# Kernel optimization log

Hardware: AMD Instinct MI355X
Metric: run time of the kernel (lower is better)

## Reference

```python
import jax, jax.numpy as jnp
import numpy as np

# LIF constants from norse.LIFParameters in the module
DT = 1e-3
TAU_MEM_INV = 4.0      # 1 / tau_mem, tau_mem = 0.25
TAU_SYN_INV = 200.0    # norse default 1/5e-3
V_TH = 0.1
ALPHA = 50.0           # super-spike surrogate slope
NHEAD = 4

@jax.custom_vjp
def spike(x):
    # SuperSpike: heaviside forward, surrogate gradient backward
    return (x > 0).astype(x.dtype)

def _spike_fwd(x):
    return spike(x), x

def _spike_bwd(x, g):
    return (g / (ALPHA * jnp.abs(x) + 1.0) ** 2,)

spike.defvjp(_spike_fwd, _spike_bwd)

def lif_reservoir(x, Win, Wres):
    # x: [B,S,I] -> spikes z: [B,S,R]. All batches start from zero state,
    # so the per-batch python loop of the original vectorizes over B.
    inp = jnp.einsum('bsi,ir->bsr', x, Win)  # precompute input currents
    B, S, R = inp.shape

    def step(carry, cur):  # cur: [B,R]
        v, i, z = carry
        total = cur + z @ Wres  # z=0 at t=0, matching the t>0 branch
        v_dec = v + DT * TAU_MEM_INV * (-v + i)  # v_leak = 0
        i_dec = i * (1.0 - DT * TAU_SYN_INV)
        z_new = spike(v_dec - V_TH)
        v_new = (1.0 - z_new) * v_dec            # v_reset = 0
        i_new = i_dec + total
        return (v_new, i_new, z_new), z_new

    init = (jnp.zeros((B, R), x.dtype),) * 3
    _, zs = jax.lax.scan(step, init, jnp.swapaxes(inp, 0, 1))
    return jnp.swapaxes(zs, 0, 1)  # [B,S,R]

def layer_norm(x, g, b, eps=1e-5):
    m = x.mean(-1, keepdims=True)
    v = ((x - m) ** 2).mean(-1, keepdims=True)
    return (x - m) / jnp.sqrt(v + eps) * g + b

def encoder_layer(x, Wqkv, bqkv, Wo, bo, g1, b1, g2, b2, W1, c1, W2, c2):
    # Post-norm TransformerEncoderLayer, relu activation, dropout=eval(0)
    B, S, D = x.shape
    dh = D // NHEAD
    qkv = x @ Wqkv.T + bqkv
    q, k, v = jnp.split(qkv, 3, axis=-1)
    rh = lambda t: t.reshape(B, S, NHEAD, dh)
    q, k, v = rh(q), rh(k), rh(v)
    scores = jnp.einsum('bqhd,bkhd->bhqk', q, k) / jnp.sqrt(jnp.asarray(dh, x.dtype))
    attn = jax.nn.softmax(scores, axis=-1)
    o = jnp.einsum('bhqk,bkhd->bqhd', attn, v).reshape(B, S, D)
    o = o @ Wo.T + bo
    x = layer_norm(x + o, g1, b1)
    ff = jax.nn.relu(x @ W1.T + c1) @ W2.T + c2
    return layer_norm(x + ff, g2, b2)

def setup_inputs() -> dict:
    key = jax.random.key(0)
    B, S, I, R, D, L, FF = 32, 1024, 8, 512, 256, 2, 1024
    ks = jax.random.split(key, 16)
    x = jax.random.normal(ks[0], (B, S, I), jnp.float32)
    Win = jax.random.normal(ks[1], (I, R), jnp.float32) * 0.1
    # sparse reservoir: density 0.2, values uniform [0,1)
    mask = (jax.random.uniform(ks[2], (R, R)) < 0.2).astype(jnp.float32)
    Wres = jax.random.uniform(ks[3], (R, R), jnp.float32) * mask
    Wread = jax.random.normal(ks[4], (D, R), jnp.float32) * 0.04
    bread = jnp.zeros((D,), jnp.float32)
    Wqkv = jax.random.normal(ks[5], (L, 3 * D, D), jnp.float32) * 0.05
    bqkv = jnp.zeros((L, 3 * D), jnp.float32)
    Wo = jax.random.normal(ks[6], (L, D, D), jnp.float32) * 0.05
    bo = jnp.zeros((L, D), jnp.float32)
    ln1_g = jnp.ones((L, D), jnp.float32)
    ln1_b = jnp.zeros((L, D), jnp.float32)
    ln2_g = jnp.ones((L, D), jnp.float32)
    ln2_b = jnp.zeros((L, D), jnp.float32)
    Wff1 = jax.random.normal(ks[7], (L, FF, D), jnp.float32) * 0.05
    bff1 = jnp.zeros((L, FF), jnp.float32)
    Wff2 = jax.random.normal(ks[8], (L, D, FF), jnp.float32) * 0.05
    bff2 = jnp.zeros((L, D), jnp.float32)
    return dict(x=x, Win=Win, Wres=Wres, Wread=Wread, bread=bread,
                Wqkv=Wqkv, bqkv=bqkv, Wo=Wo, bo=bo,
                ln1_g=ln1_g, ln1_b=ln1_b, ln2_g=ln2_g, ln2_b=ln2_b,
                Wff1=Wff1, bff1=bff1, Wff2=Wff2, bff2=bff2)

def reference(x, Win, Wres, Wread, bread, Wqkv, bqkv, Wo, bo,
              ln1_g, ln1_b, ln2_g, ln2_b, Wff1, bff1, Wff2, bff2):
    z = lif_reservoir(x, Win, Wres)          # [B,S,R] spike trains
    h = z @ Wread.T + bread                  # readout to transformer_dim
    for l in range(Wqkv.shape[0]):           # fixed small num_layers
        h = encoder_layer(h, Wqkv[l], bqkv[l], Wo[l], bo[l],
                          ln1_g[l], ln1_b[l], ln2_g[l], ln2_b[l],
                          Wff1[l], bff1[l], Wff2[l], bff2[l])
    return h
```

## Files before the change

kernel.cpp:

```cpp
#include <hip/hip_runtime.h>
#include <stdint.h>

using short8  = __attribute__((ext_vector_type(8))) short;
using floatx4 = __attribute__((ext_vector_type(4))) float;

typedef unsigned short u16;
typedef unsigned int u32;
typedef unsigned long long u64;

#define AS1(p) ((const __attribute__((address_space(1))) void*)(p))
#define AS3(p) ((__attribute__((address_space(3))) void*)(p))

__device__ __forceinline__ float bs2f(u16 u) { return __uint_as_float(((u32)u) << 16); }
__device__ __forceinline__ u16 f2bs(float f) {
  u32 x = __float_as_uint(f);
  x += 0x7FFFu + ((x >> 16) & 1u);
  return (u16)(x >> 16);
}
__device__ __forceinline__ float lo16(u32 u) { return __uint_as_float(u << 16); }
__device__ __forceinline__ float hi16(u32 u) { return __uint_as_float(u & 0xFFFF0000u); }

__global__ __launch_bounds__(256) void cvt_k(const float* __restrict__ src,
                                             u16* __restrict__ dst, int n) {
  int i = blockIdx.x * 256 + threadIdx.x;
  if (i < n) dst[i] = f2bs(src[i]);
}

__global__ __launch_bounds__(512) void inp_k(const float* __restrict__ x,
                                             const float* __restrict__ Win,
                                             float* __restrict__ inp) {
  const int row = blockIdx.x;
  const int r = threadIdx.x;
  const float* xr = x + (size_t)row * 8;
  float s = 0.f;
#pragma unroll
  for (int k = 0; k < 8; ++k) s = fmaf(Win[k * 512 + r], xr[k], s);
  inp[(size_t)row * 512 + r] = s;
}

__global__ __launch_bounds__(64) void reservoir_k(
    const float* __restrict__ inp,
    const float* __restrict__ Wres,
    u16* __restrict__ zout)
{
  const int b = blockIdx.x;
  const int c = threadIdx.x & 63;
  const float* ib = inp + (size_t)b * 524288 + c * 8;
  u16* zb = zout + (size_t)b * 524288 + c * 8;
  float v[8] = {}, ci[8] = {}, rec[8] = {};
  u32 pz = 0;
  float4 pa[8], pc[8];
#pragma unroll
  for (int u = 0; u < 8; ++u) {
    pa[u] = *(const float4*)(ib + (size_t)u * 512);
    pc[u] = *(const float4*)(ib + (size_t)u * 512 + 4);
  }
  for (int tb = 0; tb < 128; ++tb) {
    float4 na[8], nc[8];
    if (tb < 127) {
      const float* nb = ib + (size_t)(tb + 1) * 4096;
#pragma unroll
      for (int u = 0; u < 8; ++u) {
        na[u] = *(const float4*)(nb + (size_t)u * 512);
        nc[u] = *(const float4*)(nb + (size_t)u * 512 + 4);
      }
    }
#pragma unroll
    for (int u = 0; u < 8; ++u) {
      const int t = tb * 8 + u;
      const float in[8] = {pa[u].x, pa[u].y, pa[u].z, pa[u].w,
                           pc[u].x, pc[u].y, pc[u].z, pc[u].w};
      u32 nzb = 0;
      u32 zw[4];
#pragma unroll
      for (int j = 0; j < 8; ++j) {
        const float vdec = __fadd_rn(v[j], __fmul_rn(0.004f, __fadd_rn(-v[j], ci[j])));
        const int zc = (__fadd_rn(vdec, -0.1f) > 0.f) ? 1 : 0;
        v[j] = zc ? 0.f : vdec;
        nzb |= (u32)zc << j;
        ci[j] = __fadd_rn(__fmul_rn(ci[j], 0.8f), __fadd_rn(in[j], rec[j]));
        if (j & 1) zw[j >> 1] |= zc ? 0x3F800000u : 0u;
        else       zw[j >> 1]  = zc ? 0x3F80u : 0u;
      }
      *(uint4*)(zb + (size_t)t * 512) = make_uint4(zw[0], zw[1], zw[2], zw[3]);
      const u64 anyt = __ballot((nzb ^ pz) != 0);
      if (anyt) {
#pragma unroll
        for (int j = 0; j < 8; ++j) {
          const u64 nm = __ballot((nzb >> j) & 1);
          const u64 pm = __ballot((pz >> j) & 1);
          u64 on   = nm & ~pm;
          u64 offm = pm & ~nm;
          while (on) {
            const int cc = __builtin_ctzll(on); on &= on - 1;
            const float* wr = Wres + ((size_t)(cc * 8 + j) << 9) + c * 8;
            const float4 w0 = *(const float4*)wr;
            const float4 w1 = *(const float4*)(wr + 4);
            rec[0] += w0.x; rec[1] += w0.y; rec[2] += w0.z; rec[3] += w0.w;
            rec[4] += w1.x; rec[5] += w1.y; rec[6] += w1.z; rec[7] += w1.w;
          }
          while (offm) {
            const int cc = __builtin_ctzll(offm); offm &= offm - 1;
            const float* wr = Wres + ((size_t)(cc * 8 + j) << 9) + c * 8;
            const float4 w0 = *(const float4*)wr;
            const float4 w1 = *(const float4*)(wr + 4);
            rec[0] -= w0.x; rec[1] -= w0.y; rec[2] -= w0.z; rec[3] -= w0.w;
            rec[4] -= w1.x; rec[5] -= w1.y; rec[6] -= w1.z; rec[7] -= w1.w;
          }
        }
      }
      pz = nzb;
    }
    if (tb < 127) {
#pragma unroll
      for (int u = 0; u < 8; ++u) { pa[u] = na[u]; pc[u] = nc[u]; }
    }
  }
}

enum { MODE_BF16 = 0, MODE_F32 = 1, MODE_DUAL = 2, MODE_QKV = 3 };

template <int WM, int WN, int MODE>
__global__ __launch_bounds__(WM * WN * 64) void gemm_bt(
    const u16* __restrict__ A, const u16* __restrict__ B,
    const float* __restrict__ bias, void* __restrict__ C0,
    void* __restrict__ C1, void* __restrict__ C2, int K, int lda, int ldb,
    int ldc, long long sA, long long sB, long long sC, float scale, int relu)
{
  constexpr int BM = WM * 64, BN = WN * 64, BK = 32;
  constexpr int NT = WM * WN * 64;
  constexpr int CA = BM * 4 / NT, CB = BN * 4 / NT;
  __shared__ __align__(16) u16 As[BM * BK];
  __shared__ __align__(16) u16 Bs[BN * BK];
  const int tid = threadIdx.x;
  const int bz = blockIdx.z;
  const u16* Ab = A + (size_t)bz * sA + (size_t)blockIdx.y * BM * lda;
  const u16* Bb = B + (size_t)bz * sB + (size_t)blockIdx.x * BN * ldb;
  const int wavei = tid >> 6, lane = tid & 63;
  const int r16 = lane & 15, quad = lane >> 4;
  const int wm = (wavei % WM) * 64, wn = (wavei / WM) * 64;
  floatx4 acc[4][4] = {};
  for (int k0 = 0; k0 < K; k0 += BK) {
#pragma unroll
    for (int c = 0; c < CA; ++c) {
      const int idx = c * NT + tid;
      const int row = idx >> 2, kc = (idx & 3) << 3;
      __builtin_amdgcn_global_load_lds(AS1(Ab + (size_t)row * lda + k0 + kc),
                                       AS3(As + idx * 8), 16, 0, 0);
    }
#pragma unroll
    for (int c = 0; c < CB; ++c) {
      const int idx = c * NT + tid;
      const int row = idx >> 2, kc = (idx & 3) << 3;
      __builtin_amdgcn_global_load_lds(AS1(Bb + (size_t)row * ldb + k0 + kc),
                                       AS3(Bs + idx * 8), 16, 0, 0);
    }
    __syncthreads();
    short8 af[4], bfr[4];
#pragma unroll
    for (int i = 0; i < 4; ++i)
      af[i] = *(const short8*)&As[(wm + i * 16 + r16) * BK + quad * 8];
#pragma unroll
    for (int i = 0; i < 4; ++i)
      bfr[i] = *(const short8*)&Bs[(wn + i * 16 + r16) * BK + quad * 8];
#pragma unroll
    for (int i = 0; i < 4; ++i)
#pragma unroll
      for (int j = 0; j < 4; ++j)
        acc[i][j] = __builtin_amdgcn_mfma_f32_16x16x32_bf16(af[i], bfr[j], acc[i][j], 0, 0, 0);
    __syncthreads();
  }
#pragma unroll
  for (int i = 0; i < 4; ++i) {
#pragma unroll
    for (int j = 0; j < 4; ++j) {
#pragma unroll
      for (int q = 0; q < 4; ++q) {
        const int m = blockIdx.y * BM + wm + i * 16 + quad * 4 + q;
        const int n = blockIdx.x * BN + wn + j * 16 + r16;
        float val = acc[i][j][q] * scale;
        if (bias) val += bias[n];
        if (relu) val = fmaxf(val, 0.f);
        if constexpr (MODE == MODE_BF16) {
          ((u16*)C0)[(size_t)bz * sC + (size_t)m * ldc + n] = f2bs(val);
        } else if constexpr (MODE == MODE_F32) {
          ((float*)C0)[(size_t)m * ldc + n] = val;
        } else if constexpr (MODE == MODE_DUAL) {
          ((float*)C0)[(size_t)m * ldc + n] = val;
          ((u16*)C1)[(size_t)m * ldc + n] = f2bs(val);
        } else if constexpr (MODE == MODE_QKV) {
          const int b = m >> 10, s = m & 1023;
          const u16 outv = f2bs(val);
          const int h = (n & 255) >> 6, d = n & 63;
          if (n < 256)
            ((u16*)C0)[(((size_t)(b * 4 + h)) * 1024 + s) * 64 + d] = outv;
          else if (n < 512)
            ((u16*)C1)[(((size_t)(b * 4 + h)) * 1024 + s) * 64 + d] = outv;
          else
            ((u16*)C2)[(((size_t)(b * 4 + h)) * 64 + d) * 1024 + s] = outv;
        }
      }
    }
  }
}

__global__ __launch_bounds__(256) void attn_k(
    const u16* __restrict__ q_s,
    const u16* __restrict__ k_s,
    const u16* __restrict__ v_t,
    u16* __restrict__ o16)
{
  constexpr int LQ = 72, LV = 136, LP = 136;
  __shared__ __align__(16) u16 Qs[128 * LQ];
  __shared__ __align__(16) u16 Ks[128 * LQ];
  __shared__ __align__(16) u16 Vt[64 * LV];
  __shared__ __align__(16) u16 Ps[128 * LP];
  const int tid = threadIdx.x;
  const int w = tid >> 6, lane = tid & 63;
  const int r16 = lane & 15, quad = lane >> 4;
  const int p = blockIdx.y;
  const int q0 = blockIdx.x * 128;
  const u16* qg = q_s + ((size_t)p * 1024 + q0) * 64;
  const u16* kg = k_s + (size_t)p * 65536;
  const u16* vg = v_t + (size_t)p * 65536;

#pragma unroll
  for (int it = 0; it < 4; ++it) {
    const int idx = it * 256 + tid;
    const int row = idx >> 3, c8 = (idx & 7) * 8;
    *(uint4*)&Qs[row * LQ + c8] = *(const uint4*)(qg + (size_t)row * 64 + c8);
    *(uint4*)&Ks[row * LQ + c8] = *(const uint4*)(kg + (size_t)row * 64 + c8);
  }
#pragma unroll
  for (int it = 0; it < 4; ++it) {
    const int idx = it * 256 + tid;
    const int row = idx >> 4, c8 = (idx & 15) * 8;
    *(uint4*)&Vt[row * LV + c8] = *(const uint4*)(vg + (size_t)row * 1024 + c8);
  }
  __syncthreads();

  short8 aq[2][2];
#pragma unroll
  for (int i = 0; i < 2; ++i)
#pragma unroll
    for (int kc = 0; kc < 2; ++kc)
      aq[i][kc] = *(const short8*)&Qs[(w * 32 + i * 16 + r16) * LQ + kc * 32 + quad * 8];

  floatx4 o[2][4] = {};
  float mr[2][4], l[2][4];
#pragma unroll
  for (int i = 0; i < 2; ++i)
#pragma unroll
    for (int q = 0; q < 4; ++q) { mr[i][q] = -3e38f; l[i][q] = 0.f; }

  for (int kt = 0; kt < 8; ++kt) {
    uint4 kpre[4], vpre[4];
    if (kt < 7) {
      const u16* kgn = kg + (size_t)(kt + 1) * 128 * 64;
#pragma unroll
      for (int it = 0; it < 4; ++it) {
        const int idx = it * 256 + tid;
        kpre[it] = *(const uint4*)(kgn + (size_t)(idx >> 3) * 64 + (idx & 7) * 8);
        vpre[it] = *(const uint4*)(vg + (size_t)(idx >> 4) * 1024 + (kt + 1) * 128 + (idx & 15) * 8);
      }
    }
    floatx4 s[2][8] = {};
#pragma unroll
    for (int kc = 0; kc < 2; ++kc) {
#pragma unroll
      for (int f = 0; f < 8; ++f) {
        const short8 bk = *(const short8*)&Ks[(f * 16 + r16) * LQ + kc * 32 + quad * 8];
#pragma unroll
        for (int i = 0; i < 2; ++i)
          s[i][f] = __builtin_amdgcn_mfma_f32_16x16x32_bf16(aq[i][kc], bk, s[i][f], 0, 0, 0);
      }
    }
#pragma unroll
    for (int i = 0; i < 2; ++i) {
      float mt[4] = {-3e38f, -3e38f, -3e38f, -3e38f};
#pragma unroll
      for (int f = 0; f < 8; ++f)
#pragma unroll
        for (int q = 0; q < 4; ++q) {
          s[i][f][q] *= 0.125f;
          mt[q] = fmaxf(mt[q], s[i][f][q]);
        }
#pragma unroll
      for (int off = 8; off > 0; off >>= 1)
#pragma unroll
        for (int q = 0; q < 4; ++q) mt[q] = fmaxf(mt[q], __shfl_xor(mt[q], off));
      float al[4], rs[4] = {};
#pragma unroll
      for (int q = 0; q < 4; ++q) {
        const float mn = fmaxf(mr[i][q], mt[q]);
        al[q] = __expf(mr[i][q] - mn);
        mr[i][q] = mn;
      }
#pragma unroll
      for (int f = 0; f < 8; ++f)
#pragma unroll
        for (int q = 0; q < 4; ++q) {
          const float pv = __expf(s[i][f][q] - mr[i][q]);
          s[i][f][q] = pv;
          rs[q] += pv;
        }
#pragma unroll
      for (int off = 8; off > 0; off >>= 1)
#pragma unroll
        for (int q = 0; q < 4; ++q) rs[q] += __shfl_xor(rs[q], off);
#pragma unroll
      for (int q = 0; q < 4; ++q) l[i][q] = l[i][q] * al[q] + rs[q];
#pragma unroll
      for (int n = 0; n < 4; ++n)
#pragma unroll
        for (int q = 0; q < 4; ++q) o[i][n][q] *= al[q];
#pragma unroll
      for (int f = 0; f < 8; ++f)
#pragma unroll
        for (int q = 0; q < 4; ++q)
          Ps[(w * 32 + i * 16 + quad * 4 + q) * LP + f * 16 + r16] = f2bs(s[i][f][q]);
    }
#pragma unroll
    for (int kc = 0; kc < 4; ++kc) {
      short8 ap[2];
#pragma unroll
      for (int i = 0; i < 2; ++i)
        ap[i] = *(const short8*)&Ps[(w * 32 + i * 16 + r16) * LP + kc * 32 + quad * 8];
#pragma unroll
      for (int n = 0; n < 4; ++n) {
        const short8 bv = *(const short8*)&Vt[(n * 16 + r16) * LV + kc * 32 + quad * 8];
#pragma unroll
        for (int i = 0; i < 2; ++i)
          o[i][n] = __builtin_amdgcn_mfma_f32_16x16x32_bf16(ap[i], bv, o[i][n], 0, 0, 0);
      }
    }
    __syncthreads();
    if (kt < 7) {
#pragma unroll
      for (int it = 0; it < 4; ++it) {
        const int idx = it * 256 + tid;
        *(uint4*)&Ks[(idx >> 3) * LQ + (idx & 7) * 8] = kpre[it];
        *(uint4*)&Vt[(idx >> 4) * LV + (idx & 15) * 8] = vpre[it];
      }
      __syncthreads();
    }
  }
  const int bb = p >> 2, hh = p & 3;
#pragma unroll
  for (int i = 0; i < 2; ++i)
#pragma unroll
    for (int q = 0; q < 4; ++q) {
      const float inv = 1.f / l[i][q];
      const int srow = q0 + w * 32 + i * 16 + quad * 4 + q;
#pragma unroll
      for (int n = 0; n < 4; ++n)
        o16[((size_t)bb * 1024 + srow) * 256 + hh * 64 + n * 16 + r16] =
            f2bs(o[i][n][q] * inv);
    }
}

__global__ __launch_bounds__(256) void ln_k(const float* __restrict__ x,
                                            const float* __restrict__ add,
                                            const float* __restrict__ g,
                                            const float* __restrict__ bta,
                                            float* __restrict__ y32,
                                            u16* __restrict__ y16) {
  const int row = blockIdx.x * 4 + (threadIdx.x >> 6);
  const int lane = threadIdx.x & 63;
  const size_t base = (size_t)row * 256 + lane * 4;
  const float4 xv = *(const float4*)(x + base);
  const float4 av = *(const float4*)(add + base);
  float sv[4] = {xv.x + av.x, xv.y + av.y, xv.z + av.z, xv.w + av.w};
  float sum = sv[0] + sv[1] + sv[2] + sv[3];
#pragma unroll
  for (int off = 32; off > 0; off >>= 1) sum += __shfl_xor(sum, off);
  const float mean = sum * (1.f / 256.f);
  float var = 0.f;
  float d[4];
#pragma unroll
  for (int i = 0; i < 4; ++i) { d[i] = sv[i] - mean; var += d[i] * d[i]; }
#pragma unroll
  for (int off = 32; off > 0; off >>= 1) var += __shfl_xor(var, off);
  var *= (1.f / 256.f);
  const float inv = 1.f / sqrtf(var + 1e-5f);
  float yv[4];
#pragma unroll
  for (int i = 0; i < 4; ++i)
    yv[i] = d[i] * inv * g[lane * 4 + i] + bta[lane * 4 + i];
  if (y32) *(float4*)(y32 + base) = make_float4(yv[0], yv[1], yv[2], yv[3]);
  if (y16) {
    const u32 p0 = (u32)f2bs(yv[0]) | ((u32)f2bs(yv[1]) << 16);
    const u32 p1 = (u32)f2bs(yv[2]) | ((u32)f2bs(yv[3]) << 16);
    *(uint2*)(y16 + base) = make_uint2(p0, p1);
  }
}

extern "C" void kernel_launch(void* const* d_in, const int* in_sizes, int n_in,
                              void* d_out, int out_size, void* d_ws,
                              size_t ws_size, hipStream_t stream) {
  (void)in_sizes; (void)n_in; (void)out_size; (void)ws_size;
  const float* x     = (const float*)d_in[0];
  const float* Win   = (const float*)d_in[1];
  const float* Wres  = (const float*)d_in[2];
  const float* Wread = (const float*)d_in[3];
  const float* bread = (const float*)d_in[4];
  const float* Wqkv  = (const float*)d_in[5];
  const float* bqkv  = (const float*)d_in[6];
  const float* Wo    = (const float*)d_in[7];
  const float* bo    = (const float*)d_in[8];
  const float* g1    = (const float*)d_in[9];
  const float* b1    = (const float*)d_in[10];
  const float* g2    = (const float*)d_in[11];
  const float* b2    = (const float*)d_in[12];
  const float* W1    = (const float*)d_in[13];
  const float* c1    = (const float*)d_in[14];
  const float* W2    = (const float*)d_in[15];
  const float* c2    = (const float*)d_in[16];

  char* ws = (char*)d_ws;
  size_t off = 0;
  auto carve = [&](size_t bytes) {
    char* p = ws + off;
    off += (bytes + 255) & ~(size_t)255;
    return p;
  };
  u16* z      = (u16*)carve((size_t)32 * 1024 * 512 * 2);
  u16* wrd16  = (u16*)carve((size_t)256 * 512 * 2);
  u16* wqkv16 = (u16*)carve((size_t)2 * 768 * 256 * 2);
  u16* wo16   = (u16*)carve((size_t)2 * 256 * 256 * 2);
  u16* w116   = (u16*)carve((size_t)2 * 1024 * 256 * 2);
  u16* w216   = (u16*)carve((size_t)2 * 256 * 1024 * 2);
  u16* q_s    = (u16*)carve((size_t)128 * 1024 * 64 * 2);
  u16* k_s    = (u16*)carve((size_t)128 * 1024 * 64 * 2);
  u16* v_t    = (u16*)carve((size_t)128 * 64 * 1024 * 2);
  float* h32  = (float*)carve((size_t)32768 * 256 * 4);
  float* lin  = (float*)carve((size_t)32768 * 256 * 4);
  u16* h16    = (u16*)carve((size_t)32768 * 256 * 2);
  u16* ff1    = (u16*)carve((size_t)32768 * 1024 * 2);
  u16* o16    = h16;
  float* inp  = (float*)ff1;

  cvt_k<<<dim3(512), dim3(256), 0, stream>>>(Wread, wrd16, 131072);
  cvt_k<<<dim3(1536), dim3(256), 0, stream>>>(Wqkv, wqkv16, 393216);
  cvt_k<<<dim3(512), dim3(256), 0, stream>>>(Wo, wo16, 131072);
  cvt_k<<<dim3(2048), dim3(256), 0, stream>>>(W1, w116, 524288);
  cvt_k<<<dim3(2048), dim3(256), 0, stream>>>(W2, w216, 524288);

  inp_k<<<dim3(32768), dim3(512), 0, stream>>>(x, Win, inp);
  reservoir_k<<<dim3(32), dim3(64), 0, stream>>>(inp, Wres, z);

  gemm_bt<2, 2, MODE_DUAL><<<dim3(2, 256, 1), dim3(256), 0, stream>>>(
      z, wrd16, bread, h32, h16, nullptr, 512, 512, 512, 256, 0, 0, 0, 1.0f, 0);

  for (int l = 0; l < 2; ++l) {
    gemm_bt<2, 2, MODE_QKV><<<dim3(6, 256, 1), dim3(256), 0, stream>>>(
        h16, wqkv16 + (size_t)l * 196608, bqkv + l * 768, q_s, k_s, v_t, 256,
        256, 256, 0, 0, 0, 0, 1.0f, 0);
    attn_k<<<dim3(8, 128), dim3(256), 0, stream>>>(q_s, k_s, v_t, o16);
    gemm_bt<2, 2, MODE_F32><<<dim3(2, 256, 1), dim3(256), 0, stream>>>(
        o16, wo16 + (size_t)l * 65536, bo + l * 256, lin, nullptr, nullptr,
        256, 256, 256, 256, 0, 0, 0, 1.0f, 0);
    ln_k<<<dim3(8192), dim3(256), 0, stream>>>(h32, lin, g1 + l * 256,
                                               b1 + l * 256, h32, h16);
    gemm_bt<2, 2, MODE_BF16><<<dim3(8, 256, 1), dim3(256), 0, stream>>>(
        h16, w116 + (size_t)l * 262144, c1 + l * 1024, ff1, nullptr, nullptr,
        256, 256, 256, 1024, 0, 0, 0, 1.0f, 1);
    gemm_bt<2, 2, MODE_F32><<<dim3(2, 256, 1), dim3(256), 0, stream>>>(
        ff1, w216 + (size_t)l * 262144, c2 + l * 256, lin, nullptr, nullptr,
        1024, 1024, 1024, 256, 0, 0, 0, 1.0f, 0);
    float* y32 = (l == 1) ? (float*)d_out : h32;
    u16* y16 = (l == 1) ? nullptr : h16;
    ln_k<<<dim3(8192), dim3(256), 0, stream>>>(h32, lin, g2 + l * 256,
                                               b2 + l * 256, y32, y16);
  }
}
```

Before: 1.332 ms.

## Stage reservoir inputs in LDS, pack LIF math as float2, merge weight casts

The reservoir kernel now bulk-loads 32-timestep tiles of input currents into shared memory with global_load_lds, replacing the per-step register prefetch. The per-neuron LIF update uses float2 vector math with FP contraction disabled, which may map to packed FP32 instructions. The five weight-conversion launches are merged into one kernel. The tile load is followed by a full wait with no double buffering, so load latency is exposed once per tile.

```diff
diff --git a/kernel.cpp b/kernel.cpp
--- a/kernel.cpp
+++ b/kernel.cpp
@@ -20,10 +20,17 @@
 __device__ __forceinline__ float lo16(u32 u) { return __uint_as_float(u << 16); }
 __device__ __forceinline__ float hi16(u32 u) { return __uint_as_float(u & 0xFFFF0000u); }
 
-__global__ __launch_bounds__(256) void cvt_k(const float* __restrict__ src,
-                                             u16* __restrict__ dst, int n) {
-  int i = blockIdx.x * 256 + threadIdx.x;
-  if (i < n) dst[i] = f2bs(src[i]);
+__global__ __launch_bounds__(256) void cvt_all_k(
+    const float* __restrict__ s0, const float* __restrict__ s1,
+    const float* __restrict__ s2, const float* __restrict__ s3,
+    const float* __restrict__ s4, u16* __restrict__ d0, u16* __restrict__ d1,
+    u16* __restrict__ d2, u16* __restrict__ d3, u16* __restrict__ d4) {
+  const int i = blockIdx.x * 256 + threadIdx.x;
+  if (i < 131072)        d0[i] = f2bs(s0[i]);
+  else if (i < 524288)   d1[i - 131072] = f2bs(s1[i - 131072]);
+  else if (i < 655360)   d2[i - 524288] = f2bs(s2[i - 524288]);
+  else if (i < 1179648)  d3[i - 655360] = f2bs(s3[i - 655360]);
+  else                   d4[i - 1179648] = f2bs(s4[i - 1179648]);
 }
 
 __global__ __launch_bounds__(512) void inp_k(const float* __restrict__ x,
@@ -38,82 +45,82 @@
   inp[(size_t)row * 512 + r] = s;
 }
 
-__global__ __launch_bounds__(64) void reservoir_k(
+__global__ __launch_bounds__(64, 1) void reservoir_k(
     const float* __restrict__ inp,
     const float* __restrict__ Wres,
     u16* __restrict__ zout)
 {
+#pragma clang fp contract(off)
+  typedef __attribute__((ext_vector_type(2))) float f2;
   const int b = blockIdx.x;
   const int c = threadIdx.x & 63;
-  const float* ib = inp + (size_t)b * 524288 + c * 8;
+  __shared__ __align__(16) float s_in[16384];
+  const float* ib = inp + (size_t)b * 524288;
   u16* zb = zout + (size_t)b * 524288 + c * 8;
-  float v[8] = {}, ci[8] = {}, rec[8] = {};
+  f2 v[4] = {}, ci[4] = {}, rec[4] = {};
   u32 pz = 0;
-  float4 pa[8], pc[8];
-#pragma unroll
-  for (int u = 0; u < 8; ++u) {
-    pa[u] = *(const float4*)(ib + (size_t)u * 512);
-    pc[u] = *(const float4*)(ib + (size_t)u * 512 + 4);
-  }
-  for (int tb = 0; tb < 128; ++tb) {
-    float4 na[8], nc[8];
-    if (tb < 127) {
-      const float* nb = ib + (size_t)(tb + 1) * 4096;
+  for (int tile = 0; tile < 32; ++tile) {
+    const float* gt = ib + (size_t)tile * 16384;
+#pragma unroll
+    for (int i = 0; i < 64; ++i)
+      __builtin_amdgcn_global_load_lds(AS1(gt + i * 256 + c * 4),
+                                       AS3(s_in + i * 256 + c * 4), 16, 0, 0);
+    __builtin_amdgcn_s_waitcnt(0x0F70);
+    for (int tq = 0; tq < 4; ++tq) {
 #pragma unroll
       for (int u = 0; u < 8; ++u) {
-        na[u] = *(const float4*)(nb + (size_t)u * 512);
-        nc[u] = *(const float4*)(nb + (size_t)u * 512 + 4);
-      }
-    }
-#pragma unroll
-    for (int u = 0; u < 8; ++u) {
-      const int t = tb * 8 + u;
-      const float in[8] = {pa[u].x, pa[u].y, pa[u].z, pa[u].w,
-                           pc[u].x, pc[u].y, pc[u].z, pc[u].w};
-      u32 nzb = 0;
-      u32 zw[4];
-#pragma unroll
-      for (int j = 0; j < 8; ++j) {
-        const float vdec = __fadd_rn(v[j], __fmul_rn(0.004f, __fadd_rn(-v[j], ci[j])));
-        const int zc = (__fadd_rn(vdec, -0.1f) > 0.f) ? 1 : 0;
-        v[j] = zc ? 0.f : vdec;
-        nzb |= (u32)zc << j;
-        ci[j] = __fadd_rn(__fmul_rn(ci[j], 0.8f), __fadd_rn(in[j], rec[j]));
-        if (j & 1) zw[j >> 1] |= zc ? 0x3F800000u : 0u;
-        else       zw[j >> 1]  = zc ? 0x3F80u : 0u;
-      }
-      *(uint4*)(zb + (size_t)t * 512) = make_uint4(zw[0], zw[1], zw[2], zw[3]);
-      const u64 anyt = __ballot((nzb ^ pz) != 0);
-      if (anyt) {
-#pragma unroll
-        for (int j = 0; j < 8; ++j) {
-          const u64 nm = __ballot((nzb >> j) & 1);
-          const u64 pm = __ballot((pz >> j) & 1);
-          u64 on   = nm & ~pm;
-          u64 offm = pm & ~nm;
-          while (on) {
-            const int cc = __builtin_ctzll(on); on &= on - 1;
-            const float* wr = Wres + ((size_t)(cc * 8 + j) << 9) + c * 8;
-            const float4 w0 = *(const float4*)wr;
-            const float4 w1 = *(const float4*)(wr + 4);
-            rec[0] += w0.x; rec[1] += w0.y; rec[2] += w0.z; rec[3] += w0.w;
-            rec[4] += w1.x; rec[5] += w1.y; rec[6] += w1.z; rec[7] += w1.w;
-          }
-          while (offm) {
-            const int cc = __builtin_ctzll(offm); offm &= offm - 1;
-            const float* wr = Wres + ((size_t)(cc * 8 + j) << 9) + c * 8;
-            const float4 w0 = *(const float4*)wr;
-            const float4 w1 = *(const float4*)(wr + 4);
-            rec[0] -= w0.x; rec[1] -= w0.y; rec[2] -= w0.z; rec[3] -= w0.w;
-            rec[4] -= w1.x; rec[5] -= w1.y; rec[6] -= w1.z; rec[7] -= w1.w;
+        const int ts = tq * 8 + u;
+        const int t = tile * 32 + ts;
+        const float4 xa = *(const float4*)&s_in[ts * 512 + c * 8];
+        const float4 xc = *(const float4*)&s_in[ts * 512 + c * 8 + 4];
+        const f2 inx[4] = {{xa.x, xa.y}, {xa.z, xa.w},
+                           {xc.x, xc.y}, {xc.z, xc.w}};
+        u32 nzb = 0;
+        u32 zw[4];
+#pragma unroll
+        for (int j = 0; j < 4; ++j) {
+          const f2 t1 = ci[j] - v[j];
+          const f2 vdec = v[j] + t1 * 0.004f;
+          const f2 xm = vdec - 0.1f;
+          const int z0 = (xm.x > 0.f) ? 1 : 0;
+          const int z1 = (xm.y > 0.f) ? 1 : 0;
+          v[j].x = z0 ? 0.f : vdec.x;
+          v[j].y = z1 ? 0.f : vdec.y;
+          nzb |= (u32)z0 << (2 * j);
+          nzb |= (u32)z1 << (2 * j + 1);
+          const f2 t3 = inx[j] + rec[j];
+          ci[j] = ci[j] * 0.8f + t3;
+          zw[j] = (z0 ? 0x3F80u : 0u) | (z1 ? 0x3F800000u : 0u);
+        }
+        *(uint4*)(zb + (size_t)t * 512) = make_uint4(zw[0], zw[1], zw[2], zw[3]);
+        const u64 anyt = __ballot((nzb ^ pz) != 0);
+        if (anyt) {
+#pragma unroll
+          for (int j = 0; j < 8; ++j) {
+            const u64 nm = __ballot((nzb >> j) & 1);
+            const u64 pm = __ballot((pz >> j) & 1);
+            u64 on   = nm & ~pm;
+            u64 offm = pm & ~nm;
+            while (on) {
+              const int cc = __builtin_ctzll(on); on &= on - 1;
+              const float* wr = Wres + ((size_t)(cc * 8 + j) << 9) + c * 8;
+              const float4 w0 = *(const float4*)wr;
+              const float4 w1 = *(const float4*)(wr + 4);
+              rec[0] += (f2){w0.x, w0.y}; rec[1] += (f2){w0.z, w0.w};
+              rec[2] += (f2){w1.x, w1.y}; rec[3] += (f2){w1.z, w1.w};
+            }
+            while (offm) {
+              const int cc = __builtin_ctzll(offm); offm &= offm - 1;
+              const float* wr = Wres + ((size_t)(cc * 8 + j) << 9) + c * 8;
+              const float4 w0 = *(const float4*)wr;
+              const float4 w1 = *(const float4*)(wr + 4);
+              rec[0] -= (f2){w0.x, w0.y}; rec[1] -= (f2){w0.z, w0.w};
+              rec[2] -= (f2){w1.x, w1.y}; rec[3] -= (f2){w1.z, w1.w};
+            }
           }
         }
-      }
-      pz = nzb;
-    }
-    if (tb < 127) {
-#pragma unroll
-      for (int u = 0; u < 8; ++u) { pa[u] = na[u]; pc[u] = nc[u]; }
+        pz = nzb;
+      }
     }
   }
 }
@@ -440,12 +447,9 @@
   u16* o16    = h16;
   float* inp  = (float*)ff1;
 
-  cvt_k<<<dim3(512), dim3(256), 0, stream>>>(Wread, wrd16, 131072);
-  cvt_k<<<dim3(1536), dim3(256), 0, stream>>>(Wqkv, wqkv16, 393216);
-  cvt_k<<<dim3(512), dim3(256), 0, stream>>>(Wo, wo16, 131072);
-  cvt_k<<<dim3(2048), dim3(256), 0, stream>>>(W1, w116, 524288);
-  cvt_k<<<dim3(2048), dim3(256), 0, stream>>>(W2, w216, 524288);
-
+  cvt_all_k<<<dim3(6656), dim3(256), 0, stream>>>(Wread, Wqkv, Wo, W1, W2,
+                                                  wrd16, wqkv16, wo16, w116,
+                                                  w216);
   inp_k<<<dim3(32768), dim3(512), 0, stream>>>(x, Win, inp);
   reservoir_k<<<dim3(32), dim3(64), 0, stream>>>(inp, Wres, z);
 
```

Measured after the change: 1.362 ms. +2.2%, slower.
